# Kernel tuning notes

Measured on AMD Instinct MI355X. Metric: run time of the kernel, lower is better.

## Reference

```python
import jax, jax.numpy as jnp
import numpy as np

N_NODES = 50000
N_EDGES = 800000
D = 128  # node_dim == edge_dim == out_dim


def setup_inputs() -> dict:
    key = jax.random.key(0)
    ks = jax.random.split(key, 8)
    x = jax.random.normal(ks[0], (N_NODES, D), dtype=jnp.float32)
    edge_feat = jax.random.normal(ks[1], (N_EDGES, D), dtype=jnp.float32)
    src = jax.random.randint(ks[2], (N_EDGES,), 0, N_NODES)
    dst = jax.random.randint(ks[3], (N_EDGES,), 0, N_NODES)
    # xavier-ish init scales
    W_fc = jax.random.normal(ks[4], (D, D), dtype=jnp.float32) * (1.0 / np.sqrt(D))
    W_rel = jax.random.normal(ks[5], (D, 2 * D), dtype=jnp.float32) * (1.0 / np.sqrt(2 * D))
    b_rel = jnp.zeros((D,), dtype=jnp.float32)
    W_attn = jax.random.normal(ks[6], (1, 2 * D), dtype=jnp.float32) * (1.0 / np.sqrt(2 * D))
    return {"x": x, "edge_feat": edge_feat, "src": src, "dst": dst,
            "W_fc": W_fc, "W_rel": W_rel, "b_rel": b_rel, "W_attn": W_attn}


def reference(x, edge_feat, src, dst, W_fc, W_rel, b_rel, W_attn):
    n = x.shape[0]
    # z = fc(input), no bias
    z = x @ W_fc.T                                    # [N, D]
    z_src = z[src]                                    # [E, D] gather
    z_dst = z[dst]                                    # [E, D] gather
    # end = relation_fc(cat([edge_h, z_dst]))
    end = jnp.concatenate([edge_feat, z_dst], axis=1) @ W_rel.T + b_rel  # [E, D]
    # a = attn_fc(cat([z_src, end])); e = leaky_relu(a)
    a = (jnp.concatenate([z_src, end], axis=1) @ W_attn.T)[:, 0]         # [E]
    e = jax.nn.leaky_relu(a, negative_slope=0.01)
    # segment softmax over each destination node's mailbox
    m = jax.ops.segment_max(e, dst, num_segments=n)   # [N]
    ex = jnp.exp(e - m[dst])                          # [E]
    denom = jax.ops.segment_sum(ex, dst, num_segments=n)                 # [N]
    alpha = ex / denom[dst]                           # [E]
    # weighted scatter-sum of src z into dst
    h = jax.ops.segment_sum(alpha[:, None] * z_src, dst, num_segments=n)  # [N, D]
    return h
```

## Files before the change

### kernel.cpp

```cpp
#include <hip/hip_runtime.h>

#define D 128

typedef float fx4 __attribute__((ext_vector_type(4)));

__device__ __forceinline__ unsigned short f2bf(float f) {
    unsigned u = __float_as_uint(f);
    u += 0x7fffu + ((u >> 16) & 1u);
    return (unsigned short)(u >> 16);
}
__device__ __forceinline__ float bf_lo(unsigned u) { return __uint_as_float(u << 16); }
__device__ __forceinline__ float bf_hi(unsigned u) { return __uint_as_float(u & 0xffff0000u); }

__global__ __launch_bounds__(256) void g_init(
    const float* __restrict__ Wrel,
    const float* __restrict__ brel,
    const float* __restrict__ Wattn,
    float* __restrict__ gbuf,
    int* __restrict__ cnt, int N)
{
    if (blockIdx.x == 0) {
        int k = threadIdx.x;
        float acc = 0.f;
        for (int j = 0; j < 128; ++j)
            acc += Wattn[128 + j] * Wrel[j * 256 + k];
        gbuf[k] = acc;
        if (k == 0) {
            float c = 0.f;
            for (int j = 0; j < 128; ++j) c += Wattn[128 + j] * brel[j];
            gbuf[256] = c;
        }
    } else {
        int i = (blockIdx.x - 1) * 256 + threadIdx.x;
        if (i < N) cnt[i] = 0;
    }
}

__global__ __launch_bounds__(256) void zgemm_pq_count(
    const float* __restrict__ x, const float* __restrict__ W,
    const float* __restrict__ attn, const float* __restrict__ gbuf,
    unsigned short* __restrict__ zb, float* __restrict__ pbuf,
    float* __restrict__ qbuf, int nrows,
    const int* __restrict__ dst, int* __restrict__ cnt, int E, int nzb)
{
    __shared__ float xs[64][132];
    __shared__ float ws[128][132];
    int tid = threadIdx.x;

    if (blockIdx.x >= nzb) {
        int e = (blockIdx.x - nzb) * 256 + tid;
        if (e < E) atomicAdd(&cnt[dst[e]], 1);
        return;
    }
    int row0 = blockIdx.x * 64;

    for (int i = tid; i < 128 * 32; i += 256) {
        int c = i >> 5, k4 = (i & 31) << 2;
        float4 v = *(const float4*)&W[c * 128 + k4];
        *(float4*)&ws[c][k4] = v;
    }
    for (int i = tid; i < 64 * 32; i += 256) {
        int r = i >> 5, k4 = (i & 31) << 2;
        int gr = row0 + r;
        float4 v = make_float4(0.f, 0.f, 0.f, 0.f);
        if (gr < nrows) v = *(const float4*)&x[(size_t)gr * D + k4];
        *(float4*)&xs[r][k4] = v;
    }
    __syncthreads();

    int tx = tid & 15, ty = tid >> 4;
    float acc[4][8] = {};
    for (int k = 0; k < 128; k += 4) {
        float4 xv[4], wv[8];
#pragma unroll
        for (int i = 0; i < 4; ++i) xv[i] = *(const float4*)&xs[ty * 4 + i][k];
#pragma unroll
        for (int j = 0; j < 8; ++j) wv[j] = *(const float4*)&ws[tx + 16 * j][k];
#pragma unroll
        for (int i = 0; i < 4; ++i)
#pragma unroll
            for (int j = 0; j < 8; ++j)
                acc[i][j] += xv[i].x * wv[j].x + xv[i].y * wv[j].y +
                             xv[i].z * wv[j].z + xv[i].w * wv[j].w;
    }

    float a1[8], g2[8];
#pragma unroll
    for (int j = 0; j < 8; ++j) {
        a1[j] = attn[tx + 16 * j];
        g2[j] = gbuf[128 + tx + 16 * j];
    }
#pragma unroll
    for (int i = 0; i < 4; ++i) {
        int gr = row0 + ty * 4 + i;
        if (gr >= nrows) continue;
        float ps = 0.f, qs = 0.f;
#pragma unroll
        for (int j = 0; j < 8; ++j) {
            zb[(size_t)gr * D + tx + 16 * j] = f2bf(acc[i][j]);
            ps += a1[j] * acc[i][j];
            qs += g2[j] * acc[i][j];
        }
#pragma unroll
        for (int off = 8; off >= 1; off >>= 1) {
            ps += __shfl_xor(ps, off);
            qs += __shfl_xor(qs, off);
        }
        if (tx == 0) { pbuf[gr] = ps; qbuf[gr] = qs; }
    }
}

__global__ __launch_bounds__(256) void fused_scan(
    const int* __restrict__ cnt, int* __restrict__ offs,
    int* __restrict__ cursor, int N, int E)
{
    __shared__ int ws_[4];
    int tid = threadIdx.x, lane = tid & 63, wid = tid >> 6;

    int limit = blockIdx.x * 1024;
    int s = 0;
    for (int i = tid; i < limit; i += 256) s += cnt[i];
#pragma unroll
    for (int off = 32; off >= 1; off >>= 1) s += __shfl_xor(s, off);
    if (lane == 0) ws_[wid] = s;
    __syncthreads();
    int prefix = ws_[0] + ws_[1] + ws_[2] + ws_[3];
    __syncthreads();

    int i0 = blockIdx.x * 1024 + tid * 4;
    int v[4];
    int tsum = 0;
#pragma unroll
    for (int j = 0; j < 4; ++j) {
        v[j] = (i0 + j < N) ? cnt[i0 + j] : 0;
        tsum += v[j];
    }
    int incl = tsum;
#pragma unroll
    for (int off = 1; off < 64; off <<= 1) {
        int t = __shfl_up(incl, off);
        if (lane >= off) incl += t;
    }
    if (lane == 63) ws_[wid] = incl;
    __syncthreads();
    int woff = 0;
    for (int w = 0; w < wid; ++w) woff += ws_[w];
    int run = prefix + woff + incl - tsum;
#pragma unroll
    for (int j = 0; j < 4; ++j) {
        if (i0 + j < N) { offs[i0 + j] = run; cursor[i0 + j] = run; }
        run += v[j];
    }
    if (blockIdx.x == 0 && tid == 0) offs[N] = E;
}

__global__ __launch_bounds__(256) void edge_logits_scatter(
    const float* __restrict__ ef,
    const int* __restrict__ src, const int* __restrict__ dst,
    const float* __restrict__ gbuf,
    const float* __restrict__ pbuf, const float* __restrict__ qbuf,
    int* __restrict__ cursor, int2* __restrict__ spack, int E)
{
    int tid = threadIdx.x;
    int lane = tid & 15;
    int e = blockIdx.x * 16 + (tid >> 4);
    if (e >= E) return;
    const float* efr = ef + (size_t)e * D;
    float acc = 0.f;
#pragma unroll
    for (int p = 0; p < 2; ++p) {
        int idx = lane * 4 + p * 64;
        fx4 a4  = __builtin_nontemporal_load((const fx4*)&efr[idx]);
        float4 g14 = *(const float4*)&gbuf[idx];
        acc += a4.x * g14.x + a4.y * g14.y + a4.z * g14.z + a4.w * g14.w;
    }
#pragma unroll
    for (int off = 8; off >= 1; off >>= 1) acc += __shfl_xor(acc, off);
    if (lane == 0) {
        int s = src[e], d = dst[e];
        float a = acc + pbuf[s] + qbuf[d] + gbuf[256];
        float ev = a > 0.f ? a : 0.01f * a;
        int pos = atomicAdd(&cursor[d], 1);
        spack[pos] = make_int2(s, __float_as_int(__expf(ev)));
    }
}

__global__ __launch_bounds__(256) void node_gather(
    const unsigned short* __restrict__ zb, const int2* __restrict__ spack,
    const int* __restrict__ offs, float* __restrict__ out, int N)
{
    int tid = threadIdx.x, half = tid & 31;
    int node = blockIdx.x * 8 + (tid >> 5);
    if (node >= N) return;
    int o0 = offs[node], o1 = offs[node + 1];
    float4 acc = make_float4(0.f, 0.f, 0.f, 0.f);
    float denom = 0.f;
    int j = o0;
    for (; j + 1 < o1; j += 2) {
        int2 p0 = spack[j], p1 = spack[j + 1];
        uint2 u0 = *(const uint2*)&zb[(size_t)p0.x * D + half * 4];
        uint2 u1 = *(const uint2*)&zb[(size_t)p1.x * D + half * 4];
        float x0 = __int_as_float(p0.y), x1 = __int_as_float(p1.y);
        denom += x0 + x1;
        acc.x += x0 * bf_lo(u0.x) + x1 * bf_lo(u1.x);
        acc.y += x0 * bf_hi(u0.x) + x1 * bf_hi(u1.x);
        acc.z += x0 * bf_lo(u0.y) + x1 * bf_lo(u1.y);
        acc.w += x0 * bf_hi(u0.y) + x1 * bf_hi(u1.y);
    }
    if (j < o1) {
        int2 p0 = spack[j];
        uint2 u0 = *(const uint2*)&zb[(size_t)p0.x * D + half * 4];
        float x0 = __int_as_float(p0.y);
        denom += x0;
        acc.x += x0 * bf_lo(u0.x);
        acc.y += x0 * bf_hi(u0.x);
        acc.z += x0 * bf_lo(u0.y);
        acc.w += x0 * bf_hi(u0.y);
    }
    if (o1 > o0) {
        float inv = 1.f / denom;
        acc.x *= inv; acc.y *= inv; acc.z *= inv; acc.w *= inv;
    }
    *(float4*)&out[(size_t)node * D + half * 4] = acc;
}

extern "C" void kernel_launch(void* const* d_in, const int* in_sizes, int n_in,
                              void* d_out, int out_size, void* d_ws, size_t ws_size,
                              hipStream_t stream) {
    const float* x     = (const float*)d_in[0];
    const float* ef    = (const float*)d_in[1];
    const int*   src   = (const int*)d_in[2];
    const int*   dst   = (const int*)d_in[3];
    const float* Wfc   = (const float*)d_in[4];
    const float* Wrel  = (const float*)d_in[5];
    const float* brel  = (const float*)d_in[6];
    const float* Wattn = (const float*)d_in[7];
    int N = in_sizes[0] / D;
    int E = in_sizes[2];
    int nb  = (N + 1023) / 1024;
    int nzb = (N + 63) / 64;
    float* out = (float*)d_out;

    unsigned short* zb = (unsigned short*)d_ws;
    int2*  spack  = (int2*)(zb + (size_t)N * D);
    float* pbuf   = (float*)(spack + E);
    float* qbuf   = pbuf + N;
    int*   cnt    = (int*)(qbuf + N);
    int*   cursor = cnt + N;
    int*   offs   = cursor + N;
    float* gbuf   = (float*)(offs + N + 16);

    g_init<<<1 + (N + 255) / 256, 256, 0, stream>>>(Wrel, brel, Wattn, gbuf,
                                                    cnt, N);
    zgemm_pq_count<<<nzb + (E + 255) / 256, 256, 0, stream>>>(
        x, Wfc, Wattn, gbuf, zb, pbuf, qbuf, N, dst, cnt, E, nzb);
    fused_scan<<<nb, 256, 0, stream>>>(cnt, offs, cursor, N, E);
    edge_logits_scatter<<<(E + 15) / 16, 256, 0, stream>>>(ef, src, dst, gbuf,
                                                           pbuf, qbuf, cursor,
                                                           spack, E);
    node_gather<<<(N + 7) / 8, 256, 0, stream>>>(zb, spack, offs, out, N);
}
```

Measured before the change: 256.7 us.

## Bucket edge CSR by source-node chunk to improve gather locality

Edges are now counted, scanned and scattered into buckets keyed by (src chunk, dst), where a src chunk is 8192 nodes. The node gather walks each chunk's segment in turn, so concurrent reads of bf16 z rows should fall into a smaller window that stays cache-resident. In exchange the count, cursor and offset arrays grow several-fold, and the scan's per-block prefix loop re-reads a much larger array. The gather also does several offset lookups per node. The output write becomes a nontemporal store.

Result: slower. 417.5 us (+62.6%).

```diff
diff --git a/kernel.cpp b/kernel.cpp
--- a/kernel.cpp
+++ b/kernel.cpp
@@ -1,6 +1,7 @@
 #include <hip/hip_runtime.h>
 
 #define D 128
+#define CSHIFT 13
 
 typedef float fx4 __attribute__((ext_vector_type(4)));
 
@@ -17,7 +18,7 @@
     const float* __restrict__ brel,
     const float* __restrict__ Wattn,
     float* __restrict__ gbuf,
-    int* __restrict__ cnt, int N)
+    int* __restrict__ cnt, int M)
 {
     if (blockIdx.x == 0) {
         int k = threadIdx.x;
@@ -32,7 +33,7 @@
         }
     } else {
         int i = (blockIdx.x - 1) * 256 + threadIdx.x;
-        if (i < N) cnt[i] = 0;
+        if (i < M) cnt[i] = 0;
     }
 }
 
@@ -41,7 +42,8 @@
     const float* __restrict__ attn, const float* __restrict__ gbuf,
     unsigned short* __restrict__ zb, float* __restrict__ pbuf,
     float* __restrict__ qbuf, int nrows,
-    const int* __restrict__ dst, int* __restrict__ cnt, int E, int nzb)
+    const int* __restrict__ src, const int* __restrict__ dst,
+    int* __restrict__ cnt, int E, int nzb)
 {
     __shared__ float xs[64][132];
     __shared__ float ws[128][132];
@@ -49,7 +51,7 @@
 
     if (blockIdx.x >= nzb) {
         int e = (blockIdx.x - nzb) * 256 + tid;
-        if (e < E) atomicAdd(&cnt[dst[e]], 1);
+        if (e < E) atomicAdd(&cnt[(src[e] >> CSHIFT) * nrows + dst[e]], 1);
         return;
     }
     int row0 = blockIdx.x * 64;
@@ -112,7 +114,7 @@
 
 __global__ __launch_bounds__(256) void fused_scan(
     const int* __restrict__ cnt, int* __restrict__ offs,
-    int* __restrict__ cursor, int N, int E)
+    int* __restrict__ cursor, int M, int E)
 {
     __shared__ int ws_[4];
     int tid = threadIdx.x, lane = tid & 63, wid = tid >> 6;
@@ -132,7 +134,7 @@
     int tsum = 0;
 #pragma unroll
     for (int j = 0; j < 4; ++j) {
-        v[j] = (i0 + j < N) ? cnt[i0 + j] : 0;
+        v[j] = (i0 + j < M) ? cnt[i0 + j] : 0;
         tsum += v[j];
     }
     int incl = tsum;
@@ -148,10 +150,10 @@
     int run = prefix + woff + incl - tsum;
 #pragma unroll
     for (int j = 0; j < 4; ++j) {
-        if (i0 + j < N) { offs[i0 + j] = run; cursor[i0 + j] = run; }
+        if (i0 + j < M) { offs[i0 + j] = run; cursor[i0 + j] = run; }
         run += v[j];
     }
-    if (blockIdx.x == 0 && tid == 0) offs[N] = E;
+    if (blockIdx.x == 0 && tid == 0) offs[M] = E;
 }
 
 __global__ __launch_bounds__(256) void edge_logits_scatter(
@@ -159,7 +161,7 @@
     const int* __restrict__ src, const int* __restrict__ dst,
     const float* __restrict__ gbuf,
     const float* __restrict__ pbuf, const float* __restrict__ qbuf,
-    int* __restrict__ cursor, int2* __restrict__ spack, int E)
+    int* __restrict__ cursor, int2* __restrict__ spack, int E, int N)
 {
     int tid = threadIdx.x;
     int lane = tid & 15;
@@ -180,48 +182,52 @@
         int s = src[e], d = dst[e];
         float a = acc + pbuf[s] + qbuf[d] + gbuf[256];
         float ev = a > 0.f ? a : 0.01f * a;
-        int pos = atomicAdd(&cursor[d], 1);
+        int pos = atomicAdd(&cursor[(s >> CSHIFT) * N + d], 1);
         spack[pos] = make_int2(s, __float_as_int(__expf(ev)));
     }
 }
 
 __global__ __launch_bounds__(256) void node_gather(
     const unsigned short* __restrict__ zb, const int2* __restrict__ spack,
-    const int* __restrict__ offs, float* __restrict__ out, int N)
+    const int* __restrict__ offs, float* __restrict__ out, int N, int nch)
 {
     int tid = threadIdx.x, half = tid & 31;
     int node = blockIdx.x * 8 + (tid >> 5);
     if (node >= N) return;
-    int o0 = offs[node], o1 = offs[node + 1];
     float4 acc = make_float4(0.f, 0.f, 0.f, 0.f);
     float denom = 0.f;
-    int j = o0;
-    for (; j + 1 < o1; j += 2) {
-        int2 p0 = spack[j], p1 = spack[j + 1];
-        uint2 u0 = *(const uint2*)&zb[(size_t)p0.x * D + half * 4];
-        uint2 u1 = *(const uint2*)&zb[(size_t)p1.x * D + half * 4];
-        float x0 = __int_as_float(p0.y), x1 = __int_as_float(p1.y);
-        denom += x0 + x1;
-        acc.x += x0 * bf_lo(u0.x) + x1 * bf_lo(u1.x);
-        acc.y += x0 * bf_hi(u0.x) + x1 * bf_hi(u1.x);
-        acc.z += x0 * bf_lo(u0.y) + x1 * bf_lo(u1.y);
-        acc.w += x0 * bf_hi(u0.y) + x1 * bf_hi(u1.y);
-    }
-    if (j < o1) {
-        int2 p0 = spack[j];
-        uint2 u0 = *(const uint2*)&zb[(size_t)p0.x * D + half * 4];
-        float x0 = __int_as_float(p0.y);
-        denom += x0;
-        acc.x += x0 * bf_lo(u0.x);
-        acc.y += x0 * bf_hi(u0.x);
-        acc.z += x0 * bf_lo(u0.y);
-        acc.w += x0 * bf_hi(u0.y);
-    }
-    if (o1 > o0) {
+    for (int c = 0; c < nch; ++c) {
+        int o0 = offs[c * N + node], o1 = offs[c * N + node + 1];
+        int j = o0;
+        for (; j + 1 < o1; j += 2) {
+            int2 p0 = spack[j], p1 = spack[j + 1];
+            uint2 u0 = *(const uint2*)&zb[(size_t)p0.x * D + half * 4];
+            uint2 u1 = *(const uint2*)&zb[(size_t)p1.x * D + half * 4];
+            float x0 = __int_as_float(p0.y), x1 = __int_as_float(p1.y);
+            denom += x0 + x1;
+            acc.x += x0 * bf_lo(u0.x) + x1 * bf_lo(u1.x);
+            acc.y += x0 * bf_hi(u0.x) + x1 * bf_hi(u1.x);
+            acc.z += x0 * bf_lo(u0.y) + x1 * bf_lo(u1.y);
+            acc.w += x0 * bf_hi(u0.y) + x1 * bf_hi(u1.y);
+        }
+        if (j < o1) {
+            int2 p0 = spack[j];
+            uint2 u0 = *(const uint2*)&zb[(size_t)p0.x * D + half * 4];
+            float x0 = __int_as_float(p0.y);
+            denom += x0;
+            acc.x += x0 * bf_lo(u0.x);
+            acc.y += x0 * bf_hi(u0.x);
+            acc.z += x0 * bf_lo(u0.y);
+            acc.w += x0 * bf_hi(u0.y);
+        }
+    }
+    if (denom > 0.f) {
         float inv = 1.f / denom;
         acc.x *= inv; acc.y *= inv; acc.z *= inv; acc.w *= inv;
     }
-    *(float4*)&out[(size_t)node * D + half * 4] = acc;
+    fx4 res;
+    res.x = acc.x; res.y = acc.y; res.z = acc.z; res.w = acc.w;
+    __builtin_nontemporal_store(res, (fx4*)&out[(size_t)node * D + half * 4]);
 }
 
 extern "C" void kernel_launch(void* const* d_in, const int* in_sizes, int n_in,
@@ -237,7 +243,8 @@
     const float* Wattn = (const float*)d_in[7];
     int N = in_sizes[0] / D;
     int E = in_sizes[2];
-    int nb  = (N + 1023) / 1024;
+    int nch = (N + (1 << CSHIFT) - 1) >> CSHIFT;
+    int M = nch * N;
     int nzb = (N + 63) / 64;
     float* out = (float*)d_out;
 
@@ -246,17 +253,17 @@
     float* pbuf   = (float*)(spack + E);
     float* qbuf   = pbuf + N;
     int*   cnt    = (int*)(qbuf + N);
-    int*   cursor = cnt + N;
-    int*   offs   = cursor + N;
-    float* gbuf   = (float*)(offs + N + 16);
-
-    g_init<<<1 + (N + 255) / 256, 256, 0, stream>>>(Wrel, brel, Wattn, gbuf,
-                                                    cnt, N);
+    int*   cursor = cnt + M;
+    int*   offs   = cursor + M;
+    float* gbuf   = (float*)(offs + M + 16);
+
+    g_init<<<1 + (M + 255) / 256, 256, 0, stream>>>(Wrel, brel, Wattn, gbuf,
+                                                    cnt, M);
     zgemm_pq_count<<<nzb + (E + 255) / 256, 256, 0, stream>>>(
-        x, Wfc, Wattn, gbuf, zb, pbuf, qbuf, N, dst, cnt, E, nzb);
-    fused_scan<<<nb, 256, 0, stream>>>(cnt, offs, cursor, N, E);
+        x, Wfc, Wattn, gbuf, zb, pbuf, qbuf, N, src, dst, cnt, E, nzb);
+    fused_scan<<<(M + 1023) / 1024, 256, 0, stream>>>(cnt, offs, cursor, M, E);
     edge_logits_scatter<<<(E + 15) / 16, 256, 0, stream>>>(ef, src, dst, gbuf,
                                                            pbuf, qbuf, cursor,
-                                                           spack, E);
-    node_gather<<<(N + 7) / 8, 256, 0, stream>>>(zb, spack, offs, out, N);
-}
+                                                           spack, E, N);
+    node_gather<<<(N + 7) / 8, 256, 0, stream>>>(zb, spack, offs, out, N, nch);
+}
```
